# Optimization experiments

Hardware: AMD Instinct MI355X
Metric: run time of the kernel (lower is better)

Reference implementation:

```python
import jax, jax.numpy as jnp
import numpy as np

N = 50000
E = 800000
FEAT, COND, HID, LAT = 64, 32, 64, 32


def gcn_conv(x, W, b, src, dst, n):
    xw = x @ W  # [N, out]
    deg = jnp.zeros((n,), xw.dtype).at[dst].add(1.0) + 1.0  # in-degree + self loop
    dinv = jax.lax.rsqrt(deg)
    coef = dinv[src] * dinv[dst]  # [E]
    msg = xw[src] * coef[:, None]  # gather + scale
    agg = jax.ops.segment_sum(msg, dst, num_segments=n)
    agg = agg + xw * (1.0 / deg)[:, None]  # self-loop contribution
    return agg + b


def setup_inputs() -> dict:
    key = jax.random.key(0)
    ks = jax.random.split(key, 12)
    s = 0.05
    return {
        "feature": jax.random.normal(ks[0], (N, FEAT), jnp.float32),
        "condition": jax.random.normal(ks[1], (N, COND), jnp.float32),
        "edge_index": jax.random.randint(ks[2], (2, E), 0, N, jnp.int64),
        "enc_i2h_W": jax.random.normal(ks[3], (FEAT + COND, HID), jnp.float32) * s,
        "enc_i2h_b": jnp.zeros((HID,), jnp.float32),
        "enc_mean_W": jax.random.normal(ks[4], (HID, LAT), jnp.float32) * s,
        "enc_mean_b": jnp.zeros((LAT,), jnp.float32),
        "enc_logvar_W": jax.random.normal(ks[5], (HID, LAT), jnp.float32) * s,
        "enc_logvar_b": jnp.zeros((LAT,), jnp.float32),
        "dec_i2h_W": jax.random.normal(ks[6], (LAT + COND, HID), jnp.float32) * s,
        "dec_i2h_b": jnp.zeros((HID,), jnp.float32),
        "dec_out_W": jax.random.normal(ks[7], (HID, FEAT), jnp.float32) * s,
        "dec_out_b": jnp.zeros((FEAT,), jnp.float32),
    }


def reference(feature, condition, edge_index,
              enc_i2h_W, enc_i2h_b, enc_mean_W, enc_mean_b,
              enc_logvar_W, enc_logvar_b,
              dec_i2h_W, dec_i2h_b, dec_out_W, dec_out_b):
    src, dst = edge_index[0], edge_index[1]
    n = feature.shape[0]
    # encoder
    x = jnp.concatenate([feature, condition], axis=1)
    h = jax.nn.relu(gcn_conv(x, enc_i2h_W, enc_i2h_b, src, dst, n))
    mean = gcn_conv(h, enc_mean_W, enc_mean_b, src, dst, n)
    logvar = gcn_conv(h, enc_logvar_W, enc_logvar_b, src, dst, n)
    noise = jax.random.normal(jax.random.key(42), logvar.shape, logvar.dtype)
    z = noise * jnp.exp(0.5 * logvar) + mean
    # decoder
    xd = jnp.concatenate([z, condition], axis=1)
    hd = jax.nn.relu(gcn_conv(xd, dec_i2h_W, dec_i2h_b, src, dst, n))
    out = gcn_conv(hd, dec_out_W, dec_out_b, src, dst, n)
    return (z, mean, logvar, out)
```

## Files before the change

kernel.cpp:

```cpp
#include <hip/hip_runtime.h>
#include <hip/hip_bf16.h>
#include <hip/hip_fp16.h>
#include <math.h>

typedef _Float16 f16;
typedef __attribute__((ext_vector_type(8))) _Float16 f16x8;
typedef __attribute__((ext_vector_type(4))) float f32x4;


static __device__ __forceinline__ unsigned rotl32(unsigned x, int d) {
  return (x << d) | (x >> (32 - d));
}

static __device__ __forceinline__ void threefry_0_42(unsigned& x0, unsigned& x1) {
  const unsigned ks0 = 0u, ks1 = 42u, ks2 = 0u ^ 42u ^ 0x1BD11BDAu;
  x0 += ks0; x1 += ks1;
#define TF_R(r) { x0 += x1; x1 = rotl32(x1, (r)); x1 ^= x0; }
  TF_R(13) TF_R(15) TF_R(26) TF_R(6)
  x0 += ks1; x1 += ks2 + 1u;
  TF_R(17) TF_R(29) TF_R(16) TF_R(24)
  x0 += ks2; x1 += ks0 + 2u;
  TF_R(13) TF_R(15) TF_R(26) TF_R(6)
  x0 += ks0; x1 += ks1 + 3u;
  TF_R(17) TF_R(29) TF_R(16) TF_R(24)
  x0 += ks1; x1 += ks2 + 4u;
  TF_R(13) TF_R(15) TF_R(26) TF_R(6)
  x0 += ks2; x1 += ks0 + 5u;
#undef TF_R
}

static __device__ __forceinline__ float erfinv_f(float u) {
  float w = -logf((1.0f - u) * (1.0f + u));
  float p;
  if (w < 5.0f) {
    w = w - 2.5f;
    p = 2.81022636e-08f;
    p = fmaf(p, w, 3.43273939e-07f);
    p = fmaf(p, w, -3.5233877e-06f);
    p = fmaf(p, w, -4.39150654e-06f);
    p = fmaf(p, w, 0.00021858087f);
    p = fmaf(p, w, -0.00125372503f);
    p = fmaf(p, w, -0.00417768164f);
    p = fmaf(p, w, 0.246640727f);
    p = fmaf(p, w, 1.50140941f);
  } else {
    w = sqrtf(w) - 3.0f;
    p = -0.000200214257f;
    p = fmaf(p, w, 0.000100950558f);
    p = fmaf(p, w, 0.00134934322f);
    p = fmaf(p, w, -0.00367342844f);
    p = fmaf(p, w, 0.00573950773f);
    p = fmaf(p, w, -0.0076224613f);
    p = fmaf(p, w, 0.00943887047f);
    p = fmaf(p, w, 1.00167406f);
    p = fmaf(p, w, 2.83297682f);
  }
  return p * u;
}

static __device__ __forceinline__ float jax_normal_at(unsigned j) {
  unsigned x0 = 0u, x1 = j;
  threefry_0_42(x0, x1);
  unsigned bits = x0 ^ x1;
  float f = __uint_as_float((bits >> 9) | 0x3f800000u) - 1.0f;
  float u = fmaf(f, 1.99999994f, -0.99999994f);
  return 1.41421356237f * erfinv_f(u);
}


__global__ void zero_i_kernel(int* __restrict__ p, int n) {
  int i = blockIdx.x * blockDim.x + threadIdx.x;
  if (i < n) p[i] = 0;
}

__global__ void degree_i_kernel(const int* __restrict__ dstI, int* __restrict__ cnt, int ne) {
  int e = blockIdx.x * blockDim.x + threadIdx.x;
  if (e < ne) atomicAdd(&cnt[dstI[e]], 1);
}

__global__ __launch_bounds__(256) void scan1_kernel(const int* __restrict__ cnt,
                                                    int* __restrict__ rowptr,
                                                    int* __restrict__ bsum, int n) {
  __shared__ int s[256];
  const int t = threadIdx.x;
  const int base = blockIdx.x * 1024 + t * 4;
  int v0, v1, v2, v3;
  if (base + 3 < n) {
    int4 v = *(const int4*)(cnt + base);
    v0 = v.x; v1 = v.y; v2 = v.z; v3 = v.w;
  } else {
    v0 = (base + 0 < n) ? cnt[base + 0] : 0;
    v1 = (base + 1 < n) ? cnt[base + 1] : 0;
    v2 = (base + 2 < n) ? cnt[base + 2] : 0;
    v3 = (base + 3 < n) ? cnt[base + 3] : 0;
  }
  int tot = v0 + v1 + v2 + v3;
  s[t] = tot;
  __syncthreads();
  for (int off = 1; off < 256; off <<= 1) {
    int x = (t >= off) ? s[t - off] : 0;
    __syncthreads();
    s[t] += x;
    __syncthreads();
  }
  int excl = s[t] - tot;
  if (t == 255) bsum[blockIdx.x] = s[t];
  if (base + 0 < n) rowptr[base + 0] = excl;
  if (base + 1 < n) rowptr[base + 1] = excl + v0;
  if (base + 2 < n) rowptr[base + 2] = excl + v0 + v1;
  if (base + 3 < n) rowptr[base + 3] = excl + v0 + v1 + v2;
}

__global__ __launch_bounds__(256) void scanP_kernel(int* __restrict__ bsum,
                                                    int* __restrict__ boff,
                                                    int nb, int* __restrict__ rowptr,
                                                    int n, int ne) {
  __shared__ int s[256];
  const int t = threadIdx.x;
  int v = (t < nb) ? bsum[t] : 0;
  s[t] = v;
  __syncthreads();
  for (int off = 1; off < 256; off <<= 1) {
    int x = (t >= off) ? s[t - off] : 0;
    __syncthreads();
    s[t] += x;
    __syncthreads();
  }
  if (t < nb) boff[t] = s[t] - v;
  if (t == 0) rowptr[n] = ne;
}

__global__ void scan2_kernel(int* __restrict__ rowptr, const int* __restrict__ boff,
                             int* __restrict__ cnt, float* __restrict__ dinv, int n) {
  int i = blockIdx.x * blockDim.x + threadIdx.x;
  if (i < n) {
    rowptr[i] += boff[i >> 10];
    float d = (float)cnt[i] + 1.0f;
    dinv[i] = 1.0f / sqrtf(d);
    cnt[i] = 0;
  }
}

__global__ void fill_kernel(const int* __restrict__ srcI, const int* __restrict__ dstI,
                            const int* __restrict__ rowptr, int* __restrict__ cnt,
                            unsigned short* __restrict__ ssrc, int ne) {
  int e = blockIdx.x * blockDim.x + threadIdx.x;
  if (e >= ne) return;
  int s = srcI[e], d = dstI[e];
  int pos = rowptr[d] + atomicAdd(&cnt[d], 1);
  ssrc[pos] = (unsigned short)s;
}

template<int IN1, int IN2, bool X1HALF, bool DUALW>
__global__ __launch_bounds__(256) void gemm_mfma_kernel(
    const void* __restrict__ X1v, const float* __restrict__ X2,
    const float* __restrict__ Wa, const float* __restrict__ Wb,
    const float* __restrict__ dinv, __half* __restrict__ Y, int n) {
  constexpr int IN = IN1 + IN2;
  constexpr int IP = IN + 8;
  __shared__ f16 xs[128 * IP];
  __shared__ f16 wt[64 * IP];

  const int tid = threadIdx.x;
  const int base = blockIdx.x * 128;

  for (int i = tid; i < IN * 64; i += 256) {
    int k = i >> 6, c = i & 63;
    float w;
    if (DUALW) w = (c < 32) ? Wa[k * 32 + c] : Wb[k * 32 + (c - 32)];
    else       w = Wa[i];
    wt[c * IP + k] = (f16)w;
  }
  if (X1HALF) {
    const __half* X1 = (const __half*)X1v;
    for (int idx = tid; idx < 128 * (IN1 / 8); idx += 256) {
      int node = idx / (IN1 / 8);
      int k8 = (idx % (IN1 / 8)) * 8;
      int g = base + node;
      f16x8 v = {};
      if (g < n) v = *(const f16x8*)(X1 + (size_t)g * IN1 + k8);
      *(f16x8*)&xs[node * IP + k8] = v;
    }
  } else {
    const float* X1 = (const float*)X1v;
    for (int idx = tid; idx < 128 * (IN1 / 4); idx += 256) {
      int node = idx / (IN1 / 4);
      int k4 = (idx % (IN1 / 4)) * 4;
      int g = base + node;
      float4 v = (g < n) ? *(const float4*)(X1 + (size_t)g * IN1 + k4)
                         : make_float4(0.f, 0.f, 0.f, 0.f);
      f16* p = &xs[node * IP + k4];
      p[0] = (f16)v.x; p[1] = (f16)v.y; p[2] = (f16)v.z; p[3] = (f16)v.w;
    }
  }
  if (IN2 > 0) {
    for (int idx = tid; idx < 128 * (IN2 / 4); idx += 256) {
      int node = idx / (IN2 / 4);
      int k4 = (idx % (IN2 / 4)) * 4;
      int g = base + node;
      float4 v = (g < n) ? *(const float4*)(X2 + (size_t)g * IN2 + k4)
                         : make_float4(0.f, 0.f, 0.f, 0.f);
      f16* p = &xs[node * IP + IN1 + k4];
      p[0] = (f16)v.x; p[1] = (f16)v.y; p[2] = (f16)v.z; p[3] = (f16)v.w;
    }
  }
  __syncthreads();

  const int wid  = tid >> 6;
  const int lane = tid & 63;
  const int l15  = lane & 15;
  const int lk8  = (lane >> 4) * 8;

  f32x4 acc[2][4] = {{{0.f,0.f,0.f,0.f}}};
  constexpr int KB = IN / 32;
#pragma unroll
  for (int kb = 0; kb < KB; ++kb) {
    const int k0 = kb * 32 + lk8;
    f16x8 a0 = *(const f16x8*)&xs[(wid * 32 +      l15) * IP + k0];
    f16x8 a1 = *(const f16x8*)&xs[(wid * 32 + 16 + l15) * IP + k0];
#pragma unroll
    for (int ct = 0; ct < 4; ++ct) {
      f16x8 b = *(const f16x8*)&wt[(ct * 16 + l15) * IP + k0];
      acc[0][ct] = __builtin_amdgcn_mfma_f32_16x16x32_f16(a0, b, acc[0][ct], 0, 0, 0);
      acc[1][ct] = __builtin_amdgcn_mfma_f32_16x16x32_f16(a1, b, acc[1][ct], 0, 0, 0);
    }
  }

#pragma unroll
  for (int rt = 0; rt < 2; ++rt) {
#pragma unroll
    for (int i = 0; i < 4; ++i) {
      int node = base + wid * 32 + rt * 16 + (lane >> 4) * 4 + i;
      if (node < n) {
        float dv = dinv[node];
#pragma unroll
        for (int ct = 0; ct < 4; ++ct) {
          Y[(size_t)node * 64 + ct * 16 + l15] = __float2half(acc[rt][ct][i] * dv);
        }
      }
    }
  }
}

template<int MODE>
__global__ __launch_bounds__(256) void gather_kernel(
    const int* __restrict__ rowptr, const unsigned short* __restrict__ ssrc,
    const __half* __restrict__ xwp, const float* __restrict__ dinv,
    const float* __restrict__ b0, const float* __restrict__ b1,
    void* __restrict__ outv, int n) {
  const int node = (blockIdx.x * 256 + threadIdx.x) >> 6;
  const int lane = threadIdx.x & 63;
  if (node >= n) return;
  const int hf = lane >> 5;
  const int cl = lane & 31;

  float2 a1, a2, a3, a4;
  a2.x = a2.y = a3.x = a3.y = a4.x = a4.y = 0.f;
  {
    float2 f = __half22float2(((const __half2*)(xwp + (size_t)node * 64))[cl]);
    a1.x = hf ? 0.f : f.x;
    a1.y = hf ? 0.f : f.y;
  }

  const int beg = rowptr[node];
  const int end = rowptr[node + 1];
  for (int cbase = beg; cbase < end; cbase += 64) {
    int m = end - cbase; if (m > 64) m = 64;
    unsigned sv = (lane < m) ? (unsigned)ssrc[cbase + lane] : 0u;
    int k = 0;
    for (; k + 7 < m; k += 8) {
      unsigned sa = __shfl(sv, k + 0 + hf, 64);
      unsigned sb = __shfl(sv, k + 2 + hf, 64);
      unsigned sc = __shfl(sv, k + 4 + hf, 64);
      unsigned sd = __shfl(sv, k + 6 + hf, 64);
      float2 fa = __half22float2(((const __half2*)(xwp + (size_t)sa * 64))[cl]);
      float2 fb = __half22float2(((const __half2*)(xwp + (size_t)sb * 64))[cl]);
      float2 fc = __half22float2(((const __half2*)(xwp + (size_t)sc * 64))[cl]);
      float2 fd = __half22float2(((const __half2*)(xwp + (size_t)sd * 64))[cl]);
      a1.x += fa.x; a1.y += fa.y;
      a2.x += fb.x; a2.y += fb.y;
      a3.x += fc.x; a3.y += fc.y;
      a4.x += fd.x; a4.y += fd.y;
    }
    for (; k + 1 < m; k += 2) {
      unsigned sa = __shfl(sv, k + hf, 64);
      float2 fa = __half22float2(((const __half2*)(xwp + (size_t)sa * 64))[cl]);
      a1.x += fa.x; a1.y += fa.y;
    }
    if (k < m) {
      unsigned sa = __shfl(sv, k, 64);
      if (hf == 0) {
        float2 fa = __half22float2(((const __half2*)(xwp + (size_t)sa * 64))[cl]);
        a1.x += fa.x; a1.y += fa.y;
      }
    }
  }
  float2 acc;
  acc.x = (a1.x + a2.x) + (a3.x + a4.x);
  acc.y = (a1.y + a2.y) + (a3.y + a4.y);
  acc.x += __shfl(acc.x, lane ^ 32, 64);
  acc.y += __shfl(acc.y, lane ^ 32, 64);
  float dv = dinv[node];
  float vx = acc.x * dv, vy = acc.y * dv;

  if (hf != 0) return;

  const int c0 = 2 * cl;
  if (MODE == 0) {
    __half* out = (__half*)outv;
    __half2 o = __floats2half2_rn(fmaxf(vx + b0[c0], 0.0f), fmaxf(vy + b0[c0 + 1], 0.0f));
    ((__half2*)(out + (size_t)node * 64))[cl] = o;
  } else if (MODE == 2) {
    float* out = (float*)outv;
    float2 o;
    o.x = vx + b0[c0];
    o.y = vy + b0[c0 + 1];
    ((float2*)(out + (size_t)node * 64))[cl] = o;
  } else {
    float* out = (float*)outv;
    float bx = (c0 < 32) ? b0[c0] : b1[c0 - 32];
    float by = (c0 + 1 < 32) ? b0[c0 + 1] : b1[c0 + 1 - 32];
    vx += bx; vy += by;
    float ox = __shfl(vx, lane + 16, 64);
    float oy = __shfl(vy, lane + 16, 64);
    const int NZ = n * 32;
    if (cl < 16) {
      int j = node * 32 + c0;
      float n0 = jax_normal_at((unsigned)j);
      float n1 = jax_normal_at((unsigned)(j + 1));
      out[j]     = fmaf(n0, expf(0.5f * ox), vx);
      out[j + 1] = fmaf(n1, expf(0.5f * oy), vy);
      out[NZ + j]     = vx;
      out[NZ + j + 1] = vy;
    } else {
      int j = node * 32 + (c0 - 32);
      out[2 * NZ + j]     = vx;
      out[2 * NZ + j + 1] = vy;
    }
  }
}


extern "C" void kernel_launch(void* const* d_in, const int* in_sizes, int n_in,
                              void* d_out, int out_size, void* d_ws, size_t ws_size,
                              hipStream_t stream) {
  const float* feat = (const float*)d_in[0];
  const float* cond = (const float*)d_in[1];
  const int*   eidx = (const int*)d_in[2];
  const float* W1  = (const float*)d_in[3];
  const float* b1  = (const float*)d_in[4];
  const float* Wm  = (const float*)d_in[5];
  const float* bm  = (const float*)d_in[6];
  const float* Wlv = (const float*)d_in[7];
  const float* blv = (const float*)d_in[8];
  const float* Wd  = (const float*)d_in[9];
  const float* bd  = (const float*)d_in[10];
  const float* Wo  = (const float*)d_in[11];
  const float* bo  = (const float*)d_in[12];

  const int n  = in_sizes[0] / 64;
  const int ne = in_sizes[2] / 2;
  const int* srcI = eidx;
  const int* dstI = eidx + ne;

  int*   cnt    = (int*)d_ws;
  int*   rowptr = cnt + n;
  int*   bsum   = rowptr + n + 1;
  int*   boff   = bsum + 256;
  float* dinv   = (float*)(boff + 256 + 3);
  __half* xwp   = (__half*)(dinv + n);
  __half* h     = xwp + (size_t)n * 64;
  unsigned short* ssrc = (unsigned short*)(h + (size_t)n * 64);

  float* dout   = (float*)d_out;
  float* zbuf   = dout;
  float* outbuf = dout + (size_t)3 * n * 32;

  const int BT = 256;
  auto blk = [](long long t) { return (int)((t + 255) / 256); };
  const int nb_n  = blk(n);
  const int nb_e  = blk(ne);
  const int nb_sc = (n + 1023) / 1024;
  const int nb_gw = blk((long long)n * 64);
  const int nb_g  = (n + 127) / 128;

  hipLaunchKernelGGL(zero_i_kernel, dim3(nb_n), dim3(BT), 0, stream, cnt, n);
  hipLaunchKernelGGL(degree_i_kernel, dim3(nb_e), dim3(BT), 0, stream, dstI, cnt, ne);
  hipLaunchKernelGGL(scan1_kernel, dim3(nb_sc), dim3(BT), 0, stream, cnt, rowptr, bsum, n);
  hipLaunchKernelGGL(scanP_kernel, dim3(1), dim3(BT), 0, stream, bsum, boff, nb_sc, rowptr, n, ne);
  hipLaunchKernelGGL(scan2_kernel, dim3(nb_n), dim3(BT), 0, stream, rowptr, boff, cnt, dinv, n);
  hipLaunchKernelGGL(fill_kernel, dim3(nb_e), dim3(BT), 0, stream,
                     srcI, dstI, rowptr, cnt, ssrc, ne);

  hipLaunchKernelGGL((gemm_mfma_kernel<64, 32, false, false>), dim3(nb_g), dim3(BT), 0, stream,
                     feat, cond, W1, nullptr, dinv, xwp, n);
  hipLaunchKernelGGL((gather_kernel<0>), dim3(nb_gw), dim3(BT), 0, stream,
                     rowptr, ssrc, xwp, dinv, b1, nullptr, h, n);

  hipLaunchKernelGGL((gemm_mfma_kernel<64, 0, true, true>), dim3(nb_g), dim3(BT), 0, stream,
                     h, nullptr, Wm, Wlv, dinv, xwp, n);
  hipLaunchKernelGGL((gather_kernel<1>), dim3(nb_gw), dim3(BT), 0, stream,
                     rowptr, ssrc, xwp, dinv, bm, blv, dout, n);

  hipLaunchKernelGGL((gemm_mfma_kernel<32, 32, false, false>), dim3(nb_g), dim3(BT), 0, stream,
                     zbuf, cond, Wd, nullptr, dinv, xwp, n);
  hipLaunchKernelGGL((gather_kernel<0>), dim3(nb_gw), dim3(BT), 0, stream,
                     rowptr, ssrc, xwp, dinv, bd, nullptr, h, n);

  hipLaunchKernelGGL((gemm_mfma_kernel<64, 0, true, false>), dim3(nb_g), dim3(BT), 0, stream,
                     h, nullptr, Wo, nullptr, dinv, xwp, n);
  hipLaunchKernelGGL((gather_kernel<2>), dim3(nb_gw), dim3(BT), 0, stream,
                     rowptr, ssrc, xwp, dinv, bo, nullptr, outbuf, n);
}
```

Measured before the change: 248.0 us.

## Replace atomic CSR fill with two-pass bucketed counting sort

The single scatter kernel, which did a global atomic per edge into random rows, is replaced by two passes. The first pass bins edges into 256-row buckets using shared-memory histograms and reserves one global atomic per bucket per block. The second pass places each edge into its final row slot using shared-memory atomics within its bucket. This aims to cut global atomic contention and make writes more coalesced, in exchange for an extra kernel launch and an intermediate coarse buffer. The packed format relies on node ids fitting in 16 bits and bucket ids in 8 bits, and the bucket cursor array has 256 entries, so it assumes n at most about 65536.

```diff
diff --git a/kernel.cpp b/kernel.cpp
--- a/kernel.cpp
+++ b/kernel.cpp
@@ -131,24 +131,89 @@
 }
 
 __global__ void scan2_kernel(int* __restrict__ rowptr, const int* __restrict__ boff,
-                             int* __restrict__ cnt, float* __restrict__ dinv, int n) {
+                             const int* __restrict__ cnt, float* __restrict__ dinv,
+                             int* __restrict__ bcur, int n) {
   int i = blockIdx.x * blockDim.x + threadIdx.x;
   if (i < n) {
-    rowptr[i] += boff[i >> 10];
+    int rp = rowptr[i] + boff[i >> 10];
+    rowptr[i] = rp;
+    if ((i & 255) == 0) bcur[i >> 8] = rp;
     float d = (float)cnt[i] + 1.0f;
     dinv[i] = 1.0f / sqrtf(d);
-    cnt[i] = 0;
-  }
-}
-
-__global__ void fill_kernel(const int* __restrict__ srcI, const int* __restrict__ dstI,
-                            const int* __restrict__ rowptr, int* __restrict__ cnt,
-                            unsigned short* __restrict__ ssrc, int ne) {
-  int e = blockIdx.x * blockDim.x + threadIdx.x;
-  if (e >= ne) return;
-  int s = srcI[e], d = dstI[e];
-  int pos = rowptr[d] + atomicAdd(&cnt[d], 1);
-  ssrc[pos] = (unsigned short)s;
+  }
+}
+
+#define EPB 2048
+__global__ __launch_bounds__(256) void fillA_kernel(
+    const int* __restrict__ srcI, const int* __restrict__ dstI,
+    int* __restrict__ bcur, unsigned* __restrict__ coarse, int ne) {
+  __shared__ int hist[256], hpre[256], hcur[256], gbase[256];
+  __shared__ unsigned st[EPB];
+  const int tid = threadIdx.x;
+  const int base = blockIdx.x * EPB;
+
+  hist[tid] = 0; hcur[tid] = 0;
+  __syncthreads();
+
+  int s[8], d[8];
+#pragma unroll
+  for (int k = 0; k < 8; ++k) {
+    int e = base + k * 256 + tid;
+    if (e < ne) { s[k] = srcI[e]; d[k] = dstI[e]; }
+    else        { s[k] = -1;      d[k] = 0; }
+  }
+#pragma unroll
+  for (int k = 0; k < 8; ++k)
+    if (s[k] >= 0) atomicAdd(&hist[d[k] >> 8], 1);
+  __syncthreads();
+
+  int hv = hist[tid];
+  hpre[tid] = hv;
+  __syncthreads();
+  for (int off = 1; off < 256; off <<= 1) {
+    int x = (tid >= off) ? hpre[tid - off] : 0;
+    __syncthreads();
+    hpre[tid] += x;
+    __syncthreads();
+  }
+
+#pragma unroll
+  for (int k = 0; k < 8; ++k) {
+    if (s[k] >= 0) {
+      int b = d[k] >> 8;
+      int pos = (hpre[b] - hist[b]) + atomicAdd(&hcur[b], 1);
+      st[pos] = ((unsigned)b << 24) | ((unsigned)(d[k] & 255) << 16) | (unsigned)s[k];
+    }
+  }
+  if (hist[tid] > 0) gbase[tid] = atomicAdd(&bcur[tid], hist[tid]);
+  __syncthreads();
+
+  int cntE = ne - base; if (cntE > EPB) cntE = EPB;
+  for (int i = tid; i < cntE; i += 256) {
+    unsigned v = st[i];
+    int b = v >> 24;
+    int excl = hpre[b] - hist[b];
+    coarse[gbase[b] + (i - excl)] = v & 0x00FFFFFFu;
+  }
+}
+
+__global__ __launch_bounds__(256) void fillB_kernel(
+    const unsigned* __restrict__ coarse, const int* __restrict__ rowptr,
+    unsigned short* __restrict__ ssrc, int n, int ne) {
+  __shared__ int rcur[256];
+  const int b = blockIdx.x;
+  const int r0 = b << 8;
+  const int tid = threadIdx.x;
+  if (r0 + tid < n) rcur[tid] = rowptr[r0 + tid];
+  const int e0 = rowptr[r0];
+  const int e1 = (r0 + 256 <= n) ? rowptr[r0 + 256] : ne;
+  __syncthreads();
+  for (int e = e0 + tid; e < e1; e += 256) {
+    unsigned v = coarse[e];
+    int r = (v >> 16) & 255;
+    int pos = atomicAdd(&rcur[r], 1);
+    ssrc[pos] = (unsigned short)(v & 0xFFFFu);
+  }
 }
 
 template<int IN1, int IN2, bool X1HALF, bool DUALW>
@@ -362,15 +427,18 @@
   const int ne = in_sizes[2] / 2;
   const int* srcI = eidx;
   const int* dstI = eidx + ne;
+  const int nbuck = (n + 255) >> 8;
 
   int*   cnt    = (int*)d_ws;
   int*   rowptr = cnt + n;
   int*   bsum   = rowptr + n + 1;
   int*   boff   = bsum + 256;
-  float* dinv   = (float*)(boff + 256 + 3);
+  int*   bcur   = boff + 256;
+  float* dinv   = (float*)(bcur + 256 + 3);
   __half* xwp   = (__half*)(dinv + n);
   __half* h     = xwp + (size_t)n * 64;
   unsigned short* ssrc = (unsigned short*)(h + (size_t)n * 64);
+  unsigned* coarse = (unsigned*)(ssrc + ne + (ne & 1));
 
   float* dout   = (float*)d_out;
   float* zbuf   = dout;
@@ -383,14 +451,15 @@
   const int nb_sc = (n + 1023) / 1024;
   const int nb_gw = blk((long long)n * 64);
   const int nb_g  = (n + 127) / 128;
+  const int nb_fa = (ne + EPB - 1) / EPB;
 
   hipLaunchKernelGGL(zero_i_kernel, dim3(nb_n), dim3(BT), 0, stream, cnt, n);
   hipLaunchKernelGGL(degree_i_kernel, dim3(nb_e), dim3(BT), 0, stream, dstI, cnt, ne);
   hipLaunchKernelGGL(scan1_kernel, dim3(nb_sc), dim3(BT), 0, stream, cnt, rowptr, bsum, n);
   hipLaunchKernelGGL(scanP_kernel, dim3(1), dim3(BT), 0, stream, bsum, boff, nb_sc, rowptr, n, ne);
-  hipLaunchKernelGGL(scan2_kernel, dim3(nb_n), dim3(BT), 0, stream, rowptr, boff, cnt, dinv, n);
-  hipLaunchKernelGGL(fill_kernel, dim3(nb_e), dim3(BT), 0, stream,
-                     srcI, dstI, rowptr, cnt, ssrc, ne);
+  hipLaunchKernelGGL(scan2_kernel, dim3(nb_n), dim3(BT), 0, stream, rowptr, boff, cnt, dinv, bcur, n);
+  hipLaunchKernelGGL(fillA_kernel, dim3(nb_fa), dim3(BT), 0, stream, srcI, dstI, bcur, coarse, ne);
+  hipLaunchKernelGGL(fillB_kernel, dim3(nbuck), dim3(BT), 0, stream, coarse, rowptr, ssrc, n, ne);
 
   hipLaunchKernelGGL((gemm_mfma_kernel<64, 32, false, false>), dim3(nb_g), dim3(BT), 0, stream,
                      feat, cond, W1, nullptr, dinv, xwp, n);
```

After: 232.8 us. 1.06x faster.
